# Kernel tuning notes

Hardware: AMD Instinct MI355X
Metric: run time of the kernel (lower is better)

The kernel has to match this reference:

```python
import jax, jax.numpy as jnp
import numpy as np

N_NODES = 200000
N_EDGES = 6400000
IN_FEAT = 128
HIDDEN = 16


def gcn_conv(x, W, b, row, col, n):
    # PyG GCNConv: h = X W ; out_i = sum_{(j->i)} d_j^{-1/2} d_i^{-1/2} h_j + b
    # (row = source j, col = target i; self-loops already included in row/col)
    deg = jax.ops.segment_sum(jnp.ones_like(col, dtype=x.dtype), col, num_segments=n)
    dinv = jnp.where(deg > 0, jax.lax.rsqrt(deg), jnp.zeros_like(deg))
    norm = dinv[row] * dinv[col]            # [E+N]
    h = x @ W                               # [N, out] small GEMM
    msg = norm[:, None] * h[row]            # gather over edges
    out = jax.ops.segment_sum(msg, col, num_segments=n)  # scatter-add to targets
    return out + b


def setup_inputs() -> dict:
    key = jax.random.key(0)
    k1, k2, k3, k4 = jax.random.split(key, 4)
    x = jax.random.normal(k1, (N_NODES, IN_FEAT), dtype=jnp.float32)
    edge_index = jax.random.randint(k2, (2, N_EDGES), 0, N_NODES, dtype=jnp.int32)
    # Glorot-ish init for the two linear layers
    W1 = jax.random.normal(k3, (IN_FEAT, HIDDEN), dtype=jnp.float32) / np.sqrt(IN_FEAT)
    W2 = jax.random.normal(k4, (HIDDEN, 1), dtype=jnp.float32) / np.sqrt(HIDDEN)
    b1 = jnp.zeros((HIDDEN,), dtype=jnp.float32)
    b2 = jnp.zeros((1,), dtype=jnp.float32)
    return {"x": x, "edge_index": edge_index, "W1": W1, "b1": b1, "W2": W2, "b2": b2}


def reference(x, edge_index, W1, b1, W2, b2):
    n = x.shape[0]
    # add self-loops (as PyG GCNConv does by default)
    loop = jnp.arange(n, dtype=edge_index.dtype)
    row = jnp.concatenate([edge_index[0], loop])
    col = jnp.concatenate([edge_index[1], loop])
    h = gcn_conv(x, W1, b1, row, col, n)    # [N, 16]
    h = jax.nn.relu(h)
    out = gcn_conv(h, W2, b2, row, col, n)  # [N, 1]
    return out.squeeze(-1)                  # [N]
```

## Files before the change

### kernel.cpp

```cpp
#include <hip/hip_runtime.h>
#include <hip/hip_fp16.h>

#define N_NODES 200000
#define N_EDGES 6400000
#define IN_FEAT 128
#define HIDDEN  16

#define RN 512
#define CSHIFT 9
#define NC 391
#define CAPB 18432
#define SRC_MASK 0x3FFFFu
#define SB1 8192
#define NSLOT (NC * (RN + 1))

typedef float v4f __attribute__((ext_vector_type(4)));
typedef _Float16 f16x8 __attribute__((ext_vector_type(8)));
typedef float f32x4 __attribute__((ext_vector_type(4)));


__global__ void k_init(unsigned* __restrict__ ccur) {
    int b = blockIdx.x * 256 + threadIdx.x;
    if (b < NC) ccur[b] = (unsigned)b * CAPB;
}


__global__ __launch_bounds__(512) void k_cscat(const int* __restrict__ row,
                                               const int* __restrict__ col,
                                               unsigned* __restrict__ ccur,
                                               unsigned* __restrict__ tmp1) {
    __shared__ unsigned cnt[NC], gbase[NC], lcur[NC];
    const long long e0 = (long long)blockIdx.x * SB1;
    long long rem = (long long)N_EDGES - e0;
    const int n = rem > SB1 ? SB1 : (int)rem;
    if (threadIdx.x < NC) { cnt[threadIdx.x] = 0u; lcur[threadIdx.x] = 0u; }
    __syncthreads();
    const int4* c4 = (const int4*)(col + e0);
    const int4* r4 = (const int4*)(row + e0);
    const int n4 = n / 4;
    int4 cc[4], rr[4];
    int nit = 0;
    for (int i = threadIdx.x; i < n4; i += 512, ++nit) {
        int4 v = c4[i];
        cc[nit] = v;
        rr[nit] = r4[i];
        atomicAdd(&cnt[(unsigned)v.x >> CSHIFT], 1u);
        atomicAdd(&cnt[(unsigned)v.y >> CSHIFT], 1u);
        atomicAdd(&cnt[(unsigned)v.z >> CSHIFT], 1u);
        atomicAdd(&cnt[(unsigned)v.w >> CSHIFT], 1u);
    }
    __syncthreads();
    if (threadIdx.x < NC)
        gbase[threadIdx.x] = cnt[threadIdx.x] ? atomicAdd(&ccur[threadIdx.x], cnt[threadIdx.x]) : 0u;
    __syncthreads();
    for (int it = 0; it < nit; ++it) {
        int4 c = cc[it];
        int4 r = rr[it];
        unsigned b, pos;
        b = (unsigned)c.x >> CSHIFT; pos = gbase[b] + atomicAdd(&lcur[b], 1u);
        if (pos < (b + 1u) * CAPB) tmp1[pos] = (((unsigned)c.x & (RN - 1u)) << 18) | (unsigned)r.x;
        b = (unsigned)c.y >> CSHIFT; pos = gbase[b] + atomicAdd(&lcur[b], 1u);
        if (pos < (b + 1u) * CAPB) tmp1[pos] = (((unsigned)c.y & (RN - 1u)) << 18) | (unsigned)r.y;
        b = (unsigned)c.z >> CSHIFT; pos = gbase[b] + atomicAdd(&lcur[b], 1u);
        if (pos < (b + 1u) * CAPB) tmp1[pos] = (((unsigned)c.z & (RN - 1u)) << 18) | (unsigned)r.z;
        b = (unsigned)c.w >> CSHIFT; pos = gbase[b] + atomicAdd(&lcur[b], 1u);
        if (pos < (b + 1u) * CAPB) tmp1[pos] = (((unsigned)c.w & (RN - 1u)) << 18) | (unsigned)r.w;
    }
}


__global__ __launch_bounds__(1024) void k_bsort(const unsigned* __restrict__ tmp1,
                                                const unsigned* __restrict__ ccur,
                                                unsigned* __restrict__ boffs,
                                                float* __restrict__ dinv,
                                                unsigned* __restrict__ sorted) {
    __shared__ unsigned dcnt[RN], dcur[RN], sscan[RN];
    const int r = blockIdx.x;
    const unsigned lo = (unsigned)r * CAPB;
    unsigned fill = ccur[r] - lo;
    if (fill > CAPB) fill = CAPB;
    const unsigned hi = lo + fill;
    const unsigned node0 = (unsigned)r * RN;
    const unsigned slot0 = (unsigned)r * (RN + 1);
    if (threadIdx.x < RN) dcnt[threadIdx.x] = 0u;
    __syncthreads();

    for (unsigned i = lo + threadIdx.x; i < hi; i += 1024)
        atomicAdd(&dcnt[tmp1[i] >> 18], 1u);
    __syncthreads();

    unsigned c = 0;
    if (threadIdx.x < RN) { c = dcnt[threadIdx.x]; sscan[threadIdx.x] = c; }
    __syncthreads();
    #pragma unroll
    for (int d = 1; d < RN; d <<= 1) {
        unsigned add = 0;
        if (threadIdx.x < RN && threadIdx.x >= d) add = sscan[threadIdx.x - d];
        __syncthreads();
        if (threadIdx.x < RN) sscan[threadIdx.x] += add;
        __syncthreads();
    }
    if (threadIdx.x < RN) {
        unsigned excl = sscan[threadIdx.x] - c;
        dcur[threadIdx.x] = excl;
        boffs[slot0 + threadIdx.x] = lo + excl;
        unsigned node = node0 + threadIdx.x;
        if (node < N_NODES) dinv[node] = rsqrtf((float)c + 1.0f);
    }
    if (threadIdx.x == 0) boffs[slot0 + RN] = hi;
    __syncthreads();

    unsigned i = lo + threadIdx.x;
    for (; i + 3072 < hi; i += 4096) {
        unsigned p0 = tmp1[i];
        unsigned p1 = tmp1[i + 1024];
        unsigned p2 = tmp1[i + 2048];
        unsigned p3 = tmp1[i + 3072];
        unsigned q0 = atomicAdd(&dcur[p0 >> 18], 1u);
        unsigned q1 = atomicAdd(&dcur[p1 >> 18], 1u);
        unsigned q2 = atomicAdd(&dcur[p2 >> 18], 1u);
        unsigned q3 = atomicAdd(&dcur[p3 >> 18], 1u);
        sorted[lo + q0] = p0 & SRC_MASK;
        sorted[lo + q1] = p1 & SRC_MASK;
        sorted[lo + q2] = p2 & SRC_MASK;
        sorted[lo + q3] = p3 & SRC_MASK;
    }
    for (; i < hi; i += 1024) {
        unsigned p = tmp1[i];
        unsigned pos = atomicAdd(&dcur[p >> 18], 1u);
        sorted[lo + pos] = p & SRC_MASK;
    }
}


__global__ __launch_bounds__(256) void k_gemm1(const float* __restrict__ x,
                                               const float* __restrict__ W1,
                                               const float* __restrict__ dinv,
                                               __half* __restrict__ h16) {
    const int wave = (blockIdx.x * 256 + threadIdx.x) >> 6;
    const int lane = threadIdx.x & 63;
    const int m16 = lane & 15;
    const int quad = lane >> 4;
    if (wave * 16 >= N_NODES) return;

    f16x8 bf[4];
    #pragma unroll
    for (int kb = 0; kb < 4; ++kb)
        #pragma unroll
        for (int j = 0; j < 8; ++j)
            bf[kb][j] = (_Float16)W1[(kb * 32 + quad * 8 + j) * HIDDEN + m16];

    const int node0 = wave * 16;
    const float* xrow = x + (size_t)(node0 + m16) * IN_FEAT + quad * 8;
    f32x4 acc = {0.f, 0.f, 0.f, 0.f};
    #pragma unroll
    for (int kb = 0; kb < 4; ++kb) {
        const v4f* p = (const v4f*)(xrow + kb * 32);
        v4f u0 = p[0], u1 = p[1];
        f16x8 af;
        af[0] = (_Float16)u0.x; af[1] = (_Float16)u0.y;
        af[2] = (_Float16)u0.z; af[3] = (_Float16)u0.w;
        af[4] = (_Float16)u1.x; af[5] = (_Float16)u1.y;
        af[6] = (_Float16)u1.z; af[7] = (_Float16)u1.w;
        acc = __builtin_amdgcn_mfma_f32_16x16x32_f16(af, bf[kb], acc, 0, 0, 0);
    }
    #pragma unroll
    for (int r = 0; r < 4; ++r) {
        int node = node0 + quad * 4 + r;
        h16[(size_t)node * HIDDEN + m16] = __float2half(dinv[node] * acc[r]);
    }
}


__global__ __launch_bounds__(256) void k_agg1(const unsigned* __restrict__ sorted,
                                              const unsigned* __restrict__ boffs,
                                              const uint2* __restrict__ h16v,
                                              const float* __restrict__ dinv,
                                              const float* __restrict__ b1,
                                              const float* __restrict__ W2,
                                              float* __restrict__ tp) {
    const unsigned tid = blockIdx.x * 256 + threadIdx.x;
    const unsigned node = tid >> 3;
    const int l = tid & 7;
    const int q = l & 3;
    const int eh = l >> 2;
    if (node >= N_NODES) return;

    const unsigned slot = node + (node >> CSHIFT);
    unsigned e = boffs[slot];
    const unsigned o1 = boffs[slot + 1];
    float a0 = 0.f, a1 = 0.f, a2 = 0.f, a3 = 0.f;

    unsigned nb0, nb1, nb2, nb3, nb4, nb5, nb6, nb7;
    bool have = (e + 16 <= o1);
    if (have) {
        nb0 = sorted[e +  0 + eh]; nb1 = sorted[e +  2 + eh];
        nb2 = sorted[e +  4 + eh]; nb3 = sorted[e +  6 + eh];
        nb4 = sorted[e +  8 + eh]; nb5 = sorted[e + 10 + eh];
        nb6 = sorted[e + 12 + eh]; nb7 = sorted[e + 14 + eh];
    }
    while (have) {
        unsigned cb0 = nb0, cb1 = nb1, cb2 = nb2, cb3 = nb3;
        unsigned cb4 = nb4, cb5 = nb5, cb6 = nb6, cb7 = nb7;
        e += 16;
        have = (e + 16 <= o1);
        if (have) {
            nb0 = sorted[e +  0 + eh]; nb1 = sorted[e +  2 + eh];
            nb2 = sorted[e +  4 + eh]; nb3 = sorted[e +  6 + eh];
            nb4 = sorted[e +  8 + eh]; nb5 = sorted[e + 10 + eh];
            nb6 = sorted[e + 12 + eh]; nb7 = sorted[e + 14 + eh];
        }
        uint2 v0 = h16v[(size_t)cb0 * 4 + q];
        uint2 v1 = h16v[(size_t)cb1 * 4 + q];
        uint2 v2 = h16v[(size_t)cb2 * 4 + q];
        uint2 v3 = h16v[(size_t)cb3 * 4 + q];
        uint2 v4 = h16v[(size_t)cb4 * 4 + q];
        uint2 v5 = h16v[(size_t)cb5 * 4 + q];
        uint2 v6 = h16v[(size_t)cb6 * 4 + q];
        uint2 v7 = h16v[(size_t)cb7 * 4 + q];
        float2 f, g;
        f = __half22float2(*(const __half2*)&v0.x); g = __half22float2(*(const __half2*)&v0.y);
        a0 += f.x; a1 += f.y; a2 += g.x; a3 += g.y;
        f = __half22float2(*(const __half2*)&v1.x); g = __half22float2(*(const __half2*)&v1.y);
        a0 += f.x; a1 += f.y; a2 += g.x; a3 += g.y;
        f = __half22float2(*(const __half2*)&v2.x); g = __half22float2(*(const __half2*)&v2.y);
        a0 += f.x; a1 += f.y; a2 += g.x; a3 += g.y;
        f = __half22float2(*(const __half2*)&v3.x); g = __half22float2(*(const __half2*)&v3.y);
        a0 += f.x; a1 += f.y; a2 += g.x; a3 += g.y;
        f = __half22float2(*(const __half2*)&v4.x); g = __half22float2(*(const __half2*)&v4.y);
        a0 += f.x; a1 += f.y; a2 += g.x; a3 += g.y;
        f = __half22float2(*(const __half2*)&v5.x); g = __half22float2(*(const __half2*)&v5.y);
        a0 += f.x; a1 += f.y; a2 += g.x; a3 += g.y;
        f = __half22float2(*(const __half2*)&v6.x); g = __half22float2(*(const __half2*)&v6.y);
        a0 += f.x; a1 += f.y; a2 += g.x; a3 += g.y;
        f = __half22float2(*(const __half2*)&v7.x); g = __half22float2(*(const __half2*)&v7.y);
        a0 += f.x; a1 += f.y; a2 += g.x; a3 += g.y;
    }
    if (e + 8 <= o1) {
        unsigned cb0 = sorted[e + 0 + eh], cb1 = sorted[e + 2 + eh];
        unsigned cb2 = sorted[e + 4 + eh], cb3 = sorted[e + 6 + eh];
        uint2 v0 = h16v[(size_t)cb0 * 4 + q];
        uint2 v1 = h16v[(size_t)cb1 * 4 + q];
        uint2 v2 = h16v[(size_t)cb2 * 4 + q];
        uint2 v3 = h16v[(size_t)cb3 * 4 + q];
        float2 f, g;
        f = __half22float2(*(const __half2*)&v0.x); g = __half22float2(*(const __half2*)&v0.y);
        a0 += f.x; a1 += f.y; a2 += g.x; a3 += g.y;
        f = __half22float2(*(const __half2*)&v1.x); g = __half22float2(*(const __half2*)&v1.y);
        a0 += f.x; a1 += f.y; a2 += g.x; a3 += g.y;
        f = __half22float2(*(const __half2*)&v2.x); g = __half22float2(*(const __half2*)&v2.y);
        a0 += f.x; a1 += f.y; a2 += g.x; a3 += g.y;
        f = __half22float2(*(const __half2*)&v3.x); g = __half22float2(*(const __half2*)&v3.y);
        a0 += f.x; a1 += f.y; a2 += g.x; a3 += g.y;
        e += 8;
    }
    for (; e < o1; ++e) {
        if (eh == 0) {
            unsigned s = sorted[e];
            uint2 v = h16v[(size_t)s * 4 + q];
            float2 f = __half22float2(*(const __half2*)&v.x);
            float2 g = __half22float2(*(const __half2*)&v.y);
            a0 += f.x; a1 += f.y; a2 += g.x; a3 += g.y;
        }
    }

    a0 += __shfl_xor(a0, 4, 8);
    a1 += __shfl_xor(a1, 4, 8);
    a2 += __shfl_xor(a2, 4, 8);
    a3 += __shfl_xor(a3, 4, 8);

    uint2 vs = h16v[(size_t)node * 4 + q];
    float2 s01 = __half22float2(*(const __half2*)&vs.x);
    float2 s23 = __half22float2(*(const __half2*)&vs.y);
    float di = dinv[node];
    float p0 = fmaf(di, a0 + s01.x, b1[4 * q + 0]);
    float p1 = fmaf(di, a1 + s01.y, b1[4 * q + 1]);
    float p2 = fmaf(di, a2 + s23.x, b1[4 * q + 2]);
    float p3 = fmaf(di, a3 + s23.y, b1[4 * q + 3]);
    float r = fmaxf(p0, 0.f) * W2[4 * q + 0] + fmaxf(p1, 0.f) * W2[4 * q + 1]
            + fmaxf(p2, 0.f) * W2[4 * q + 2] + fmaxf(p3, 0.f) * W2[4 * q + 3];
    r += __shfl_xor(r, 2, 8);
    r += __shfl_xor(r, 1, 8);
    if (l == 0) tp[node] = di * r;
}


__global__ __launch_bounds__(256) void k_agg2(const unsigned* __restrict__ sorted,
                                              const unsigned* __restrict__ boffs,
                                              const float* __restrict__ tp,
                                              const float* __restrict__ dinv,
                                              const float* __restrict__ b2,
                                              float* __restrict__ out) {
    const unsigned node = blockIdx.x * 256 + threadIdx.x;
    if (node >= N_NODES) return;

    const unsigned slot = node + (node >> CSHIFT);
    unsigned e = boffs[slot];
    const unsigned o1 = boffs[slot + 1];
    float acc = 0.f;

    unsigned n0, n1, n2, n3, n4, n5, n6, n7;
    bool have = (e + 8 <= o1);
    if (have) {
        n0 = sorted[e];     n1 = sorted[e + 1]; n2 = sorted[e + 2]; n3 = sorted[e + 3];
        n4 = sorted[e + 4]; n5 = sorted[e + 5]; n6 = sorted[e + 6]; n7 = sorted[e + 7];
    }
    while (have) {
        unsigned c0 = n0, c1 = n1, c2 = n2, c3 = n3, c4 = n4, c5 = n5, c6 = n6, c7 = n7;
        e += 8;
        have = (e + 8 <= o1);
        if (have) {
            n0 = sorted[e];     n1 = sorted[e + 1]; n2 = sorted[e + 2]; n3 = sorted[e + 3];
            n4 = sorted[e + 4]; n5 = sorted[e + 5]; n6 = sorted[e + 6]; n7 = sorted[e + 7];
        }
        float t0 = tp[c0], t1 = tp[c1], t2 = tp[c2], t3 = tp[c3];
        float t4 = tp[c4], t5 = tp[c5], t6 = tp[c6], t7 = tp[c7];
        acc += t0 + t1 + t2 + t3;
        acc += t4 + t5 + t6 + t7;
    }
    for (; e < o1; ++e) acc += tp[sorted[e]];

    out[node] = fmaf(dinv[node], tp[node] + acc, b2[0]);
}


extern "C" void kernel_launch(void* const* d_in, const int* in_sizes, int n_in,
                              void* d_out, int out_size, void* d_ws, size_t ws_size,
                              hipStream_t stream) {
    const float* x   = (const float*)d_in[0];
    const int*   ei  = (const int*)d_in[1];
    const float* W1  = (const float*)d_in[2];
    const float* b1  = (const float*)d_in[3];
    const float* W2  = (const float*)d_in[4];
    const float* b2  = (const float*)d_in[5];
    float* out = (float*)d_out;

    const int* row = ei;
    const int* col = ei + N_EDGES;

    unsigned* ccur   = (unsigned*)d_ws;
    unsigned* boffs  = ccur + 512;
    float*    dinv   = (float*)(boffs + NSLOT + 73);
    float*    tp     = dinv + N_NODES;
    __half*   h16    = (__half*)(tp + N_NODES);
    unsigned* tmp1   = (unsigned*)(h16 + (size_t)N_NODES * HIDDEN);
    unsigned* sorted = tmp1 + (size_t)NC * CAPB;

    k_init<<<2, 256, 0, stream>>>(ccur);
    k_cscat<<<(N_EDGES + SB1 - 1) / SB1, 512, 0, stream>>>(row, col, ccur, tmp1);
    k_bsort<<<NC, 1024, 0, stream>>>(tmp1, ccur, boffs, dinv, sorted);
    k_gemm1<<<(N_NODES / 16 + 3) / 4, 256, 0, stream>>>(x, W1, dinv, h16);
    k_agg1<<<(N_NODES * 8 + 255) / 256, 256, 0, stream>>>(sorted, boffs, (const uint2*)h16,
                                                          dinv, b1, W2, tp);
    k_agg2<<<(N_NODES + 255) / 256, 256, 0, stream>>>(sorted, boffs, tp, dinv, b2, out);
}
```

Before: 409.0 us.

## Replace global-atomic bucket scatter with per-block shared-memory bucketing and offset table

The edge bucketing kernel now counting-sorts each block's 8192 edges by destination bucket in shared memory and writes them back contiguously. A per-block table of bucket offsets replaces the global atomic bucket cursors and the init kernel. The bucket-sort kernel then gathers each bucket's pieces from all 782 block segments through that table, one segment per thread. This removes scattered global writes and global atomics in the first pass. In exchange the second pass runs a serial, latency-bound loop per thread over many small segments.

Result: slower. 478.1 us (+16.9%).

```diff
diff --git a/kernel.cpp b/kernel.cpp
--- a/kernel.cpp
+++ b/kernel.cpp
@@ -12,6 +12,8 @@
 #define CAPB 18432
 #define SRC_MASK 0x3FFFFu
 #define SB1 8192
+#define NBLK 782
+#define TW 392
 #define NSLOT (NC * (RN + 1))
 
 typedef float v4f __attribute__((ext_vector_type(4)));
@@ -19,114 +21,108 @@
 typedef float f32x4 __attribute__((ext_vector_type(4)));
 
 
-__global__ void k_init(unsigned* __restrict__ ccur) {
-    int b = blockIdx.x * 256 + threadIdx.x;
-    if (b < NC) ccur[b] = (unsigned)b * CAPB;
-}
-
-
 __global__ __launch_bounds__(512) void k_cscat(const int* __restrict__ row,
                                                const int* __restrict__ col,
-                                               unsigned* __restrict__ ccur,
+                                               unsigned short* __restrict__ table,
                                                unsigned* __restrict__ tmp1) {
-    __shared__ unsigned cnt[NC], gbase[NC], lcur[NC];
+    __shared__ unsigned cnt[512], cur[512], s[512];
+    __shared__ unsigned buf[SB1];
     const long long e0 = (long long)blockIdx.x * SB1;
     long long rem = (long long)N_EDGES - e0;
     const int n = rem > SB1 ? SB1 : (int)rem;
-    if (threadIdx.x < NC) { cnt[threadIdx.x] = 0u; lcur[threadIdx.x] = 0u; }
-    __syncthreads();
+    const int t = threadIdx.x;
+    cnt[t] = 0u;
+    __syncthreads();
+
     const int4* c4 = (const int4*)(col + e0);
-    const int4* r4 = (const int4*)(row + e0);
-    const int n4 = n / 4;
-    int4 cc[4], rr[4];
-    int nit = 0;
-    for (int i = threadIdx.x; i < n4; i += 512, ++nit) {
+    for (int i = t; i < n / 4; i += 512) {
         int4 v = c4[i];
-        cc[nit] = v;
-        rr[nit] = r4[i];
         atomicAdd(&cnt[(unsigned)v.x >> CSHIFT], 1u);
         atomicAdd(&cnt[(unsigned)v.y >> CSHIFT], 1u);
         atomicAdd(&cnt[(unsigned)v.z >> CSHIFT], 1u);
         atomicAdd(&cnt[(unsigned)v.w >> CSHIFT], 1u);
     }
     __syncthreads();
-    if (threadIdx.x < NC)
-        gbase[threadIdx.x] = cnt[threadIdx.x] ? atomicAdd(&ccur[threadIdx.x], cnt[threadIdx.x]) : 0u;
-    __syncthreads();
-    for (int it = 0; it < nit; ++it) {
-        int4 c = cc[it];
-        int4 r = rr[it];
-        unsigned b, pos;
-        b = (unsigned)c.x >> CSHIFT; pos = gbase[b] + atomicAdd(&lcur[b], 1u);
-        if (pos < (b + 1u) * CAPB) tmp1[pos] = (((unsigned)c.x & (RN - 1u)) << 18) | (unsigned)r.x;
-        b = (unsigned)c.y >> CSHIFT; pos = gbase[b] + atomicAdd(&lcur[b], 1u);
-        if (pos < (b + 1u) * CAPB) tmp1[pos] = (((unsigned)c.y & (RN - 1u)) << 18) | (unsigned)r.y;
-        b = (unsigned)c.z >> CSHIFT; pos = gbase[b] + atomicAdd(&lcur[b], 1u);
-        if (pos < (b + 1u) * CAPB) tmp1[pos] = (((unsigned)c.z & (RN - 1u)) << 18) | (unsigned)r.z;
-        b = (unsigned)c.w >> CSHIFT; pos = gbase[b] + atomicAdd(&lcur[b], 1u);
-        if (pos < (b + 1u) * CAPB) tmp1[pos] = (((unsigned)c.w & (RN - 1u)) << 18) | (unsigned)r.w;
-    }
+
+    unsigned cv = cnt[t];
+    s[t] = cv;
+    __syncthreads();
+    #pragma unroll
+    for (int d = 1; d < 512; d <<= 1) {
+        unsigned add = (t >= d) ? s[t - d] : 0u;
+        __syncthreads();
+        s[t] += add;
+        __syncthreads();
+    }
+    unsigned base = s[t] - cv;
+    cur[t] = base;
+    if (t < TW) table[(size_t)blockIdx.x * TW + t] = (unsigned short)base;
+    __syncthreads();
+
+    for (int i = t; i < n; i += 512) {
+        unsigned c = (unsigned)col[e0 + i];
+        unsigned sr = (unsigned)row[e0 + i];
+        unsigned b = c >> CSHIFT;
+        unsigned pos = atomicAdd(&cur[b], 1u);
+        buf[pos] = ((c & (RN - 1u)) << 18) | sr;
+    }
+    __syncthreads();
+
+    uint4* dst = (uint4*)(tmp1 + e0);
+    const uint4* src4 = (const uint4*)buf;
+    for (int i = t; i < n / 4; i += 512) dst[i] = src4[i];
 }
 
 
 __global__ __launch_bounds__(1024) void k_bsort(const unsigned* __restrict__ tmp1,
-                                                const unsigned* __restrict__ ccur,
+                                                const unsigned short* __restrict__ table,
                                                 unsigned* __restrict__ boffs,
                                                 float* __restrict__ dinv,
                                                 unsigned* __restrict__ sorted) {
     __shared__ unsigned dcnt[RN], dcur[RN], sscan[RN];
     const int r = blockIdx.x;
     const unsigned lo = (unsigned)r * CAPB;
-    unsigned fill = ccur[r] - lo;
-    if (fill > CAPB) fill = CAPB;
-    const unsigned hi = lo + fill;
     const unsigned node0 = (unsigned)r * RN;
     const unsigned slot0 = (unsigned)r * (RN + 1);
-    if (threadIdx.x < RN) dcnt[threadIdx.x] = 0u;
-    __syncthreads();
-
-    for (unsigned i = lo + threadIdx.x; i < hi; i += 1024)
-        atomicAdd(&dcnt[tmp1[i] >> 18], 1u);
+    const int t = threadIdx.x;
+
+    unsigned rbase = 0, rend = 0;
+    long long gbase = 0;
+    if (t < NBLK) {
+        rbase = table[(size_t)t * TW + r];
+        rend  = table[(size_t)t * TW + r + 1];
+        gbase = (long long)t * SB1;
+    }
+    if (t < RN) dcnt[t] = 0u;
+    __syncthreads();
+
+    for (unsigned j = rbase; j < rend; ++j)
+        atomicAdd(&dcnt[tmp1[gbase + j] >> 18], 1u);
     __syncthreads();
 
     unsigned c = 0;
-    if (threadIdx.x < RN) { c = dcnt[threadIdx.x]; sscan[threadIdx.x] = c; }
+    if (t < RN) { c = dcnt[t]; sscan[t] = c; }
     __syncthreads();
     #pragma unroll
     for (int d = 1; d < RN; d <<= 1) {
         unsigned add = 0;
-        if (threadIdx.x < RN && threadIdx.x >= d) add = sscan[threadIdx.x - d];
+        if (t < RN && t >= d) add = sscan[t - d];
         __syncthreads();
-        if (threadIdx.x < RN) sscan[threadIdx.x] += add;
+        if (t < RN) sscan[t] += add;
         __syncthreads();
     }
-    if (threadIdx.x < RN) {
-        unsigned excl = sscan[threadIdx.x] - c;
-        dcur[threadIdx.x] = excl;
-        boffs[slot0 + threadIdx.x] = lo + excl;
-        unsigned node = node0 + threadIdx.x;
+    if (t < RN) {
+        unsigned excl = sscan[t] - c;
+        dcur[t] = excl;
+        boffs[slot0 + t] = lo + excl;
+        unsigned node = node0 + t;
         if (node < N_NODES) dinv[node] = rsqrtf((float)c + 1.0f);
     }
-    if (threadIdx.x == 0) boffs[slot0 + RN] = hi;
-    __syncthreads();
-
-    unsigned i = lo + threadIdx.x;
-    for (; i + 3072 < hi; i += 4096) {
-        unsigned p0 = tmp1[i];
-        unsigned p1 = tmp1[i + 1024];
-        unsigned p2 = tmp1[i + 2048];
-        unsigned p3 = tmp1[i + 3072];
-        unsigned q0 = atomicAdd(&dcur[p0 >> 18], 1u);
-        unsigned q1 = atomicAdd(&dcur[p1 >> 18], 1u);
-        unsigned q2 = atomicAdd(&dcur[p2 >> 18], 1u);
-        unsigned q3 = atomicAdd(&dcur[p3 >> 18], 1u);
-        sorted[lo + q0] = p0 & SRC_MASK;
-        sorted[lo + q1] = p1 & SRC_MASK;
-        sorted[lo + q2] = p2 & SRC_MASK;
-        sorted[lo + q3] = p3 & SRC_MASK;
-    }
-    for (; i < hi; i += 1024) {
-        unsigned p = tmp1[i];
+    if (t == RN - 1) boffs[slot0 + RN] = lo + sscan[t];
+    __syncthreads();
+
+    for (unsigned j = rbase; j < rend; ++j) {
+        unsigned p = tmp1[gbase + j];
         unsigned pos = atomicAdd(&dcur[p >> 18], 1u);
         sorted[lo + pos] = p & SRC_MASK;
     }
@@ -338,17 +334,16 @@
     const int* row = ei;
     const int* col = ei + N_EDGES;
 
-    unsigned* ccur   = (unsigned*)d_ws;
-    unsigned* boffs  = ccur + 512;
-    float*    dinv   = (float*)(boffs + NSLOT + 73);
+    unsigned short* table = (unsigned short*)d_ws;
+    unsigned* boffs  = (unsigned*)d_ws + 153280;
+    float*    dinv   = (float*)(boffs + NSLOT + 57);
     float*    tp     = dinv + N_NODES;
     __half*   h16    = (__half*)(tp + N_NODES);
     unsigned* tmp1   = (unsigned*)(h16 + (size_t)N_NODES * HIDDEN);
-    unsigned* sorted = tmp1 + (size_t)NC * CAPB;
-
-    k_init<<<2, 256, 0, stream>>>(ccur);
-    k_cscat<<<(N_EDGES + SB1 - 1) / SB1, 512, 0, stream>>>(row, col, ccur, tmp1);
-    k_bsort<<<NC, 1024, 0, stream>>>(tmp1, ccur, boffs, dinv, sorted);
+    unsigned* sorted = tmp1 + (size_t)NBLK * SB1;
+
+    k_cscat<<<NBLK, 512, 0, stream>>>(row, col, table, tmp1);
+    k_bsort<<<NC, 1024, 0, stream>>>(tmp1, table, boffs, dinv, sorted);
     k_gemm1<<<(N_NODES / 16 + 3) / 4, 256, 0, stream>>>(x, W1, dinv, h16);
     k_agg1<<<(N_NODES * 8 + 255) / 256, 256, 0, stream>>>(sorted, boffs, (const uint2*)h16,
                                                           dinv, b1, W2, tp);
```

## Stage bucket scatter through LDS for coalesced global writes in edge binning

Applied to the files above, without the earlier changes.

The coarse scatter kernel now counts bucket sizes, scans them in shared memory, and locally sorts the block's edges into an LDS buffer by bucket. It then writes them to global memory in bucket-contiguous runs, replacing scattered per-edge global writes. This is meant to cut uncoalesced write traffic, at the cost of more shared memory (about 50KB), extra scan barriers and a second read of col/row. The fine sort kernel's main loop is also unrolled from 4 to 8 loads per iteration to get more memory-level parallelism.

After: 373.6 us. 8.6% less time.

```diff
diff --git a/kernel.cpp b/kernel.cpp
--- a/kernel.cpp
+++ b/kernel.cpp
@@ -12,6 +12,7 @@
 #define CAPB 18432
 #define SRC_MASK 0x3FFFFu
 #define SB1 8192
+#define NBLK 782
 #define NSLOT (NC * (RN + 1))
 
 typedef float v4f __attribute__((ext_vector_type(4)));
@@ -29,42 +30,55 @@
                                                const int* __restrict__ col,
                                                unsigned* __restrict__ ccur,
                                                unsigned* __restrict__ tmp1) {
-    __shared__ unsigned cnt[NC], gbase[NC], lcur[NC];
+    __shared__ unsigned cnt[512], s[512], cur[512], gdst[512];
+    __shared__ unsigned buf[SB1];
+    __shared__ unsigned short bkt[SB1];
     const long long e0 = (long long)blockIdx.x * SB1;
     long long rem = (long long)N_EDGES - e0;
     const int n = rem > SB1 ? SB1 : (int)rem;
-    if (threadIdx.x < NC) { cnt[threadIdx.x] = 0u; lcur[threadIdx.x] = 0u; }
-    __syncthreads();
+    const int t = threadIdx.x;
+    cnt[t] = 0u;
+    __syncthreads();
+
     const int4* c4 = (const int4*)(col + e0);
-    const int4* r4 = (const int4*)(row + e0);
-    const int n4 = n / 4;
-    int4 cc[4], rr[4];
-    int nit = 0;
-    for (int i = threadIdx.x; i < n4; i += 512, ++nit) {
+    for (int i = t; i < n / 4; i += 512) {
         int4 v = c4[i];
-        cc[nit] = v;
-        rr[nit] = r4[i];
         atomicAdd(&cnt[(unsigned)v.x >> CSHIFT], 1u);
         atomicAdd(&cnt[(unsigned)v.y >> CSHIFT], 1u);
         atomicAdd(&cnt[(unsigned)v.z >> CSHIFT], 1u);
         atomicAdd(&cnt[(unsigned)v.w >> CSHIFT], 1u);
     }
     __syncthreads();
-    if (threadIdx.x < NC)
-        gbase[threadIdx.x] = cnt[threadIdx.x] ? atomicAdd(&ccur[threadIdx.x], cnt[threadIdx.x]) : 0u;
-    __syncthreads();
-    for (int it = 0; it < nit; ++it) {
-        int4 c = cc[it];
-        int4 r = rr[it];
-        unsigned b, pos;
-        b = (unsigned)c.x >> CSHIFT; pos = gbase[b] + atomicAdd(&lcur[b], 1u);
-        if (pos < (b + 1u) * CAPB) tmp1[pos] = (((unsigned)c.x & (RN - 1u)) << 18) | (unsigned)r.x;
-        b = (unsigned)c.y >> CSHIFT; pos = gbase[b] + atomicAdd(&lcur[b], 1u);
-        if (pos < (b + 1u) * CAPB) tmp1[pos] = (((unsigned)c.y & (RN - 1u)) << 18) | (unsigned)r.y;
-        b = (unsigned)c.z >> CSHIFT; pos = gbase[b] + atomicAdd(&lcur[b], 1u);
-        if (pos < (b + 1u) * CAPB) tmp1[pos] = (((unsigned)c.z & (RN - 1u)) << 18) | (unsigned)r.z;
-        b = (unsigned)c.w >> CSHIFT; pos = gbase[b] + atomicAdd(&lcur[b], 1u);
-        if (pos < (b + 1u) * CAPB) tmp1[pos] = (((unsigned)c.w & (RN - 1u)) << 18) | (unsigned)r.w;
+
+    unsigned cv = cnt[t];
+    s[t] = cv;
+    __syncthreads();
+    #pragma unroll
+    for (int d = 1; d < 512; d <<= 1) {
+        unsigned add = (t >= d) ? s[t - d] : 0u;
+        __syncthreads();
+        s[t] += add;
+        __syncthreads();
+    }
+    cur[t] = s[t] - cv;
+    __syncthreads();
+
+    for (int i = t; i < n; i += 512) {
+        unsigned c = (unsigned)col[e0 + i];
+        unsigned sr = (unsigned)row[e0 + i];
+        unsigned b = c >> CSHIFT;
+        unsigned pos = atomicAdd(&cur[b], 1u);
+        buf[pos] = ((c & (RN - 1u)) << 18) | sr;
+        bkt[pos] = (unsigned short)b;
+    }
+    if (t < NC) gdst[t] = cnt[t] ? atomicAdd(&ccur[t], cnt[t]) : 0u;
+    __syncthreads();
+
+    for (int i = t; i < n; i += 512) {
+        unsigned b = bkt[i];
+        unsigned base = s[b] - cnt[b];
+        unsigned dest = gdst[b] + ((unsigned)i - base);
+        if (dest < (b + 1u) * CAPB) tmp1[dest] = buf[i];
     }
 }
 
@@ -111,19 +125,31 @@
     __syncthreads();
 
     unsigned i = lo + threadIdx.x;
-    for (; i + 3072 < hi; i += 4096) {
+    for (; i + 7168 < hi; i += 8192) {
         unsigned p0 = tmp1[i];
         unsigned p1 = tmp1[i + 1024];
         unsigned p2 = tmp1[i + 2048];
         unsigned p3 = tmp1[i + 3072];
+        unsigned p4 = tmp1[i + 4096];
+        unsigned p5 = tmp1[i + 5120];
+        unsigned p6 = tmp1[i + 6144];
+        unsigned p7 = tmp1[i + 7168];
         unsigned q0 = atomicAdd(&dcur[p0 >> 18], 1u);
         unsigned q1 = atomicAdd(&dcur[p1 >> 18], 1u);
         unsigned q2 = atomicAdd(&dcur[p2 >> 18], 1u);
         unsigned q3 = atomicAdd(&dcur[p3 >> 18], 1u);
+        unsigned q4 = atomicAdd(&dcur[p4 >> 18], 1u);
+        unsigned q5 = atomicAdd(&dcur[p5 >> 18], 1u);
+        unsigned q6 = atomicAdd(&dcur[p6 >> 18], 1u);
+        unsigned q7 = atomicAdd(&dcur[p7 >> 18], 1u);
         sorted[lo + q0] = p0 & SRC_MASK;
         sorted[lo + q1] = p1 & SRC_MASK;
         sorted[lo + q2] = p2 & SRC_MASK;
         sorted[lo + q3] = p3 & SRC_MASK;
+        sorted[lo + q4] = p4 & SRC_MASK;
+        sorted[lo + q5] = p5 & SRC_MASK;
+        sorted[lo + q6] = p6 & SRC_MASK;
+        sorted[lo + q7] = p7 & SRC_MASK;
     }
     for (; i < hi; i += 1024) {
         unsigned p = tmp1[i];
@@ -347,7 +373,7 @@
     unsigned* sorted = tmp1 + (size_t)NC * CAPB;
 
     k_init<<<2, 256, 0, stream>>>(ccur);
-    k_cscat<<<(N_EDGES + SB1 - 1) / SB1, 512, 0, stream>>>(row, col, ccur, tmp1);
+    k_cscat<<<NBLK, 512, 0, stream>>>(row, col, ccur, tmp1);
     k_bsort<<<NC, 1024, 0, stream>>>(tmp1, ccur, boffs, dinv, sorted);
     k_gemm1<<<(N_NODES / 16 + 3) / 4, 256, 0, stream>>>(x, W1, dinv, h16);
     k_agg1<<<(N_NODES * 8 + 255) / 256, 256, 0, stream>>>(sorted, boffs, (const uint2*)h16,
```
